# Kernel optimization log

Measured on AMD Instinct MI355X. Metric: run time of the kernel, lower is better.

Reference implementation:

```python
import jax, jax.numpy as jnp
import numpy as np

DIM = 1024
N_HEADS = 16
HEAD_DIM = DIM // N_HEADS
SCALE = HEAD_DIM ** -0.5


def setup_inputs() -> dict:
    key = jax.random.key(0)
    ks = jax.random.split(key, 5)
    B, N = 2, 2048
    x = jax.random.normal(ks[0], (B, N, DIM), dtype=jnp.float32)
    # torch Linear: y = x @ W.T + b, W shape (out, in)
    qkv_w = jax.random.normal(ks[1], (3 * DIM, DIM), dtype=jnp.float32) * (DIM ** -0.5)
    qkv_b = jax.random.normal(ks[2], (3 * DIM,), dtype=jnp.float32) * 0.02
    proj_w = jax.random.normal(ks[3], (DIM, DIM), dtype=jnp.float32) * (DIM ** -0.5)
    proj_b = jax.random.normal(ks[4], (DIM,), dtype=jnp.float32) * 0.02
    return {"x": x, "qkv_w": qkv_w, "qkv_b": qkv_b, "proj_w": proj_w, "proj_b": proj_b}


def reference(x, qkv_w, qkv_b, proj_w, proj_b):
    B, N, D = x.shape
    qkv = x @ qkv_w.T + qkv_b                      # [B, N, 3D]
    qkv = qkv.reshape(B, N, 3, N_HEADS, HEAD_DIM)
    qkv = jnp.transpose(qkv, (2, 0, 3, 1, 4))      # [3, B, H, N, hd]
    q, k, v = qkv[0], qkv[1], qkv[2]
    dp = jnp.einsum('bhqd,bhkd->bhqk', q, k) * SCALE  # [B, H, N, N]
    attn = jax.nn.softmax(dp, axis=-1)
    wa = jnp.einsum('bhqk,bhkd->bhqd', attn, v)    # [B, H, N, hd]
    wa = jnp.transpose(wa, (0, 2, 1, 3)).reshape(B, N, D)
    return wa @ proj_w.T + proj_b
```

## Files before the change

kernel.cpp:

```cpp
#include <hip/hip_runtime.h>

#define BATCH 2
#define SEQ   2048
#define DIM   1024
#define NHEAD 16
#define HD    64
#define BH    (BATCH * NHEAD)
#define SCALE 0.125f
#define LOG2E 1.44269504f
#define NT    (SEQ / 64)

typedef __attribute__((ext_vector_type(8))) short short8;
typedef __attribute__((ext_vector_type(4))) float f32x4;

#define MFMA16(a, b, c) __builtin_amdgcn_mfma_f32_16x16x32_bf16(a, b, c, 0, 0, 0)

__device__ __forceinline__ ushort f2bf(float f) {
    union { float f; unsigned u; } v;
    v.f = f;
    unsigned r = (v.u + 0x7FFF + ((v.u >> 16) & 1)) >> 16;
    return (ushort)r;
}

__device__ __forceinline__ uint4 ld8f_bf16(const float* p) {
    float4 f0 = *(const float4*)p;
    float4 f1 = *(const float4*)(p + 4);
    union { ushort us[8]; uint4 v; } u;
    u.us[0] = f2bf(f0.x); u.us[1] = f2bf(f0.y);
    u.us[2] = f2bf(f0.z); u.us[3] = f2bf(f0.w);
    u.us[4] = f2bf(f1.x); u.us[5] = f2bf(f1.y);
    u.us[6] = f2bf(f1.z); u.us[7] = f2bf(f1.w);
    return u.v;
}

__device__ __forceinline__ void gl_lds16(const ushort* g, ushort* l) {
    __builtin_amdgcn_global_load_lds(
        (const __attribute__((address_space(1))) unsigned int*)g,
        (__attribute__((address_space(3))) unsigned int*)l,
        16, 0, 0);
}

#define N_X  (BATCH * SEQ * DIM)
#define N_QW (3 * DIM * DIM)
#define N_PW (DIM * DIM)

__global__ __launch_bounds__(256) void cvt_kernel(
    const float* __restrict__ x, const float* __restrict__ qw,
    const float* __restrict__ pw, ushort* __restrict__ xb,
    ushort* __restrict__ qwb, ushort* __restrict__ pwb)
{
    const int i = (blockIdx.x * 256 + threadIdx.x) * 8;
    if (i < N_X)  *(uint4*)(xb  + i) = ld8f_bf16(x  + i);
    if (i < N_QW) *(uint4*)(qwb + i) = ld8f_bf16(qw + i);
    if (i < N_PW) *(uint4*)(pwb + i) = ld8f_bf16(pw + i);
}

template <int MODE, int WM, typename TOUT>
__global__ __launch_bounds__(256, 2) void gemm_bt(
    const ushort* __restrict__ A, const ushort* __restrict__ W,
    const float* __restrict__ bias, TOUT* __restrict__ out,
    int M, int Nout, int K)
{
    constexpr int BM = 2 * WM * 16;
    __shared__ __align__(16) ushort As[2][BM * 32];
    __shared__ __align__(16) ushort Bs[2][128 * 32];

    const int tid  = threadIdx.x;
    const int wave = tid >> 6, lane = tid & 63;
    const int quad = lane >> 4, l16 = lane & 15;
    const int wm = wave >> 1, wn = wave & 1;
    const int m0 = blockIdx.y * BM, n0 = blockIdx.x * 128;

    const int c0 = tid, c1 = tid + 256;
    const ushort* gA0 = A + (size_t)(m0 + (c0 >> 2)) * K + (c0 & 3) * 8;
    const ushort* gA1 = A + (size_t)(m0 + (c1 >> 2)) * K + (c1 & 3) * 8;
    const ushort* gB0 = W + (size_t)(n0 + (c0 >> 2)) * K + (c0 & 3) * 8;
    const ushort* gB1 = W + (size_t)(n0 + (c1 >> 2)) * K + (c1 & 3) * 8;

#define STAGE_G(buf, k0)                                                  \
    {                                                                     \
        gl_lds16(gA0 + (k0), &As[buf][(wave * 64) * 8]);                  \
        if (WM == 4) gl_lds16(gA1 + (k0), &As[buf][(wave * 64 + 256) * 8]); \
        gl_lds16(gB0 + (k0), &Bs[buf][(wave * 64) * 8]);                  \
        gl_lds16(gB1 + (k0), &Bs[buf][(wave * 64 + 256) * 8]);            \
    }

    f32x4 acc[WM][4];
#pragma unroll
    for (int i = 0; i < WM; i++)
#pragma unroll
        for (int j = 0; j < 4; j++) acc[i][j] = (f32x4){0.f, 0.f, 0.f, 0.f};

    const int KT = K >> 5;
    STAGE_G(0, 0)

    for (int kt = 0; kt < KT; kt++) {
        const int cur = kt & 1;
        __syncthreads();
        if (kt + 1 < KT) STAGE_G(cur ^ 1, (kt + 1) * 32)

        short8 af[WM], bfr[4];
#pragma unroll
        for (int mt = 0; mt < WM; mt++)
            af[mt] = *(const short8*)&As[cur][(wm * (WM * 16) + mt * 16 + l16) * 32 + quad * 8];
#pragma unroll
        for (int nt = 0; nt < 4; nt++)
            bfr[nt] = *(const short8*)&Bs[cur][(wn * 64 + nt * 16 + l16) * 32 + quad * 8];
#pragma unroll
        for (int mt = 0; mt < WM; mt++)
#pragma unroll
            for (int nt = 0; nt < 4; nt++)
                acc[mt][nt] = MFMA16(af[mt], bfr[nt], acc[mt][nt]);
    }

#pragma unroll
    for (int nt = 0; nt < 4; nt++) {
        const int n = n0 + wn * 64 + nt * 16 + l16;
        const float bv = bias[n];
#pragma unroll
        for (int mt = 0; mt < WM; mt++) {
            const int mBase = m0 + wm * (WM * 16) + mt * 16 + quad * 4;
#pragma unroll
            for (int r = 0; r < 4; r++) {
                const int m = mBase + r;
                float v = acc[mt][nt][r] + bv;
                if (MODE == 0) {
                    const int which = n >> 10, rem = n & 1023;
                    const int h = rem >> 6, d = rem & 63;
                    const int b = m >> 11, nq = m & 2047;
                    const int bh = b * NHEAD + h;
                    if (which == 0) v *= (SCALE * LOG2E);
                    size_t idx;
                    if (which == 2)
                        idx = (size_t)2 * BH * SEQ * HD + ((size_t)bh * HD + d) * SEQ + nq;
                    else
                        idx = (size_t)which * BH * SEQ * HD + ((size_t)bh * SEQ + nq) * HD + d;
                    ((ushort*)out)[idx] = f2bf(v);
                } else {
                    ((float*)out)[(size_t)m * Nout + n] = v;
                }
            }
        }
    }
#undef STAGE_G
}

#define PSTR 72

__global__ __launch_bounds__(512, 4) void attn_kernel(
    const ushort* __restrict__ qkv, ushort* __restrict__ wa)
{
    __shared__ __align__(16) ushort Ks[2][64 * 64];
    __shared__ __align__(16) ushort Vs[2][64 * 64];
    __shared__ __align__(16) ushort Pb[8][16 * PSTR];

    const int tid  = threadIdx.x;
    const int wave = tid >> 6, lane = tid & 63;
    const int quad = lane >> 4, l16 = lane & 15;

    const int l = blockIdx.x;
    const int bh = (l & 7) + 8 * (l >> 7);
    const int qi = (l >> 3) & 15;
    const int b = bh >> 4, h = bh & 15;

    const size_t hOff = (size_t)bh * SEQ * HD;
    const ushort* Q  = qkv + hOff;
    const ushort* Kg = qkv + (size_t)BH * SEQ * HD + hOff;
    const ushort* Vt = qkv + (size_t)2 * BH * SEQ * HD + hOff;
    const int q0 = qi * 128 + wave * 16;

    short8 aq0 = *(const short8*)&Q[(size_t)(q0 + l16) * HD + quad * 8];
    short8 aq1 = *(const short8*)&Q[(size_t)(q0 + l16) * HD + 32 + quad * 8];

    f32x4 o[4];
#pragma unroll
    for (int dt = 0; dt < 4; dt++) o[dt] = (f32x4){0.f, 0.f, 0.f, 0.f};
    float lsum[4];
#pragma unroll
    for (int r = 0; r < 4; r++) lsum[r] = 0.f;

    ushort* Pw = &Pb[wave][0];

    const int rr = lane >> 3;
    const int cc = ((lane & 7) ^ rr) * 8;
    const ushort* KgL = Kg + rr * HD + cc;
    const ushort* VtL = Vt + (size_t)rr * SEQ + cc;

#define STAGE(buf, kt)                                                       \
    {                                                                        \
        gl_lds16(KgL + (size_t)((kt) * 64 + wave * 8) * HD,                  \
                 &Ks[buf][wave * 512]);                                      \
        gl_lds16(VtL + (size_t)(wave * 8) * SEQ + (kt) * 64,                 \
                 &Vs[buf][wave * 512]);                                      \
    }

    STAGE(0, 0)

    const int sw  = (l16 & 7);
    const int ko0 = (quad ^ sw) * 8;
    const int ko1 = ko0 ^ 32;

    for (int kt = 0; kt < NT; kt++) {
        const int cur = kt & 1;
        __syncthreads();
        if (kt + 1 < NT) STAGE(cur ^ 1, kt + 1)

        f32x4 s[4];
#pragma unroll
        for (int t = 0; t < 4; t++) {
            const ushort* kb = &Ks[cur][(t * 16 + l16) * 64];
            short8 bk0 = *(const short8*)&kb[ko0];
            short8 bk1 = *(const short8*)&kb[ko1];
            f32x4 z = (f32x4){0.f, 0.f, 0.f, 0.f};
            z = MFMA16(aq0, bk0, z);
            z = MFMA16(aq1, bk1, z);
            s[t] = z;
        }

#pragma unroll
        for (int t = 0; t < 4; t++)
#pragma unroll
            for (int r = 0; r < 4; r++) {
                const float pv = __builtin_amdgcn_exp2f(s[t][r]);
                s[t][r] = pv;
                lsum[r] += pv;
            }

        short8 bv[4][2];
#pragma unroll
        for (int dt = 0; dt < 4; dt++) {
            const ushort* vb = &Vs[cur][(dt * 16 + l16) * 64];
            bv[dt][0] = *(const short8*)&vb[ko0];
            bv[dt][1] = *(const short8*)&vb[ko1];
        }

        __builtin_amdgcn_fence(__ATOMIC_ACQ_REL, "workgroup");
#pragma unroll
        for (int t = 0; t < 4; t++)
#pragma unroll
            for (int r = 0; r < 4; r++)
                Pw[(quad * 4 + r) * PSTR + l16 + t * 16] = f2bf(s[t][r]);
        __builtin_amdgcn_fence(__ATOMIC_ACQ_REL, "workgroup");

        short8 pa0 = *(const short8*)&Pw[l16 * PSTR + quad * 8];
        short8 pa1 = *(const short8*)&Pw[l16 * PSTR + 32 + quad * 8];

#pragma unroll
        for (int dt = 0; dt < 4; dt++) {
            o[dt] = MFMA16(pa0, bv[dt][0], o[dt]);
            o[dt] = MFMA16(pa1, bv[dt][1], o[dt]);
        }
    }

#pragma unroll
    for (int r = 0; r < 4; r++) {
        float ssum = lsum[r];
        ssum += __shfl_xor(ssum, 1);
        ssum += __shfl_xor(ssum, 2);
        ssum += __shfl_xor(ssum, 4);
        ssum += __shfl_xor(ssum, 8);
        lsum[r] = ssum;
    }

#pragma unroll
    for (int r = 0; r < 4; r++) {
        const float inv = 1.f / lsum[r];
        const int qrow = q0 + quad * 4 + r;
        ushort* dst = wa + ((size_t)(b * SEQ + qrow)) * DIM + h * HD;
#pragma unroll
        for (int dt = 0; dt < 4; dt++)
            dst[dt * 16 + l16] = f2bf(o[dt][r] * inv);
    }
}

extern "C" void kernel_launch(void* const* d_in, const int* in_sizes, int n_in,
                              void* d_out, int out_size, void* d_ws, size_t ws_size,
                              hipStream_t stream)
{
    const float* x      = (const float*)d_in[0];
    const float* qkv_w  = (const float*)d_in[1];
    const float* qkv_b  = (const float*)d_in[2];
    const float* proj_w = (const float*)d_in[3];
    const float* proj_b = (const float*)d_in[4];
    float* out = (float*)d_out;

    ushort* xb  = (ushort*)d_ws;
    ushort* qwb = xb  + (size_t)N_X;
    ushort* pwb = qwb + (size_t)N_QW;
    ushort* qkv = pwb + (size_t)N_PW;
    ushort* wa  = qkv + (size_t)3 * BH * SEQ * HD;

    const int M = BATCH * SEQ;
    dim3 blk(256);

    cvt_kernel<<<dim3((N_X / 8 + 255) / 256), blk, 0, stream>>>(
        x, qkv_w, proj_w, xb, qwb, pwb);

    gemm_bt<0, 4, ushort><<<dim3((3 * DIM) / 128, M / 128), blk, 0, stream>>>(
        xb, qwb, qkv_b, qkv, M, 3 * DIM, DIM);

    attn_kernel<<<dim3(512), dim3(512), 0, stream>>>(qkv, wa);

    gemm_bt<1, 2, float><<<dim3(DIM / 128, M / 64), blk, 0, stream>>>(
        wa, pwb, proj_b, out, M, DIM, DIM);
}
```

Measured before the change: 196.3 us.

## Rewrite attention with 32x32 MFMA, register-resident P via permlane swap

The attention kernel now computes transposed scores S^T = K·Q^T with 32x32x16 bf16 MFMAs, so each wave handles 32 query rows, and blocks shrink from 512 to 256 threads. The exponentiated probabilities are packed to bf16 in registers and rearranged with permlane32_swap to feed the PV MFMA directly. This removes the per-tile LDS round-trip for P and its fences. K/V tiles are staged 128 keys at a time, and s_setprio is placed around the MFMA bursts. The kernel keeps more accumulator registers live per wave and may run at lower occupancy.

```diff
diff --git a/kernel.cpp b/kernel.cpp
--- a/kernel.cpp
+++ b/kernel.cpp
@@ -8,12 +8,15 @@
 #define BH    (BATCH * NHEAD)
 #define SCALE 0.125f
 #define LOG2E 1.44269504f
-#define NT    (SEQ / 64)
+#define NT128 (SEQ / 128)
 
 typedef __attribute__((ext_vector_type(8))) short short8;
 typedef __attribute__((ext_vector_type(4))) float f32x4;
+typedef __attribute__((ext_vector_type(16))) float f32x16;
+typedef __attribute__((ext_vector_type(2))) unsigned int uint2v;
 
 #define MFMA16(a, b, c) __builtin_amdgcn_mfma_f32_16x16x32_bf16(a, b, c, 0, 0, 0)
+#define MFMA32(a, b, c) __builtin_amdgcn_mfma_f32_32x32x16_bf16(a, b, c, 0, 0, 0)
 
 __device__ __forceinline__ ushort f2bf(float f) {
     union { float f; unsigned u; } v;
@@ -145,132 +148,134 @@
 #undef STAGE_G
 }
 
-#define PSTR 72
-
-__global__ __launch_bounds__(512, 4) void attn_kernel(
+__global__ __launch_bounds__(256, 2) void attn_kernel(
     const ushort* __restrict__ qkv, ushort* __restrict__ wa)
 {
-    __shared__ __align__(16) ushort Ks[2][64 * 64];
-    __shared__ __align__(16) ushort Vs[2][64 * 64];
-    __shared__ __align__(16) ushort Pb[8][16 * PSTR];
+    __shared__ __align__(16) ushort Ks[2][2][64 * 64];
+    __shared__ __align__(16) ushort Vs[2][2][64 * 64];
 
     const int tid  = threadIdx.x;
     const int wave = tid >> 6, lane = tid & 63;
-    const int quad = lane >> 4, l16 = lane & 15;
+    const int l31  = lane & 31, hb = lane >> 5;
 
     const int l = blockIdx.x;
     const int bh = (l & 7) + 8 * (l >> 7);
     const int qi = (l >> 3) & 15;
-    const int b = bh >> 4, h = bh & 15;
+    const int b = bh >> 4, head = bh & 15;
 
     const size_t hOff = (size_t)bh * SEQ * HD;
     const ushort* Q  = qkv + hOff;
     const ushort* Kg = qkv + (size_t)BH * SEQ * HD + hOff;
     const ushort* Vt = qkv + (size_t)2 * BH * SEQ * HD + hOff;
-    const int q0 = qi * 128 + wave * 16;
-
-    short8 aq0 = *(const short8*)&Q[(size_t)(q0 + l16) * HD + quad * 8];
-    short8 aq1 = *(const short8*)&Q[(size_t)(q0 + l16) * HD + 32 + quad * 8];
-
-    f32x4 o[4];
-#pragma unroll
-    for (int dt = 0; dt < 4; dt++) o[dt] = (f32x4){0.f, 0.f, 0.f, 0.f};
-    float lsum[4];
-#pragma unroll
-    for (int r = 0; r < 4; r++) lsum[r] = 0.f;
-
-    ushort* Pw = &Pb[wave][0];
+    const int q0 = qi * 128 + wave * 32;
+
+    short8 qf[4];
+#pragma unroll
+    for (int i = 0; i < 4; i++)
+        qf[i] = *(const short8*)&Q[(size_t)(q0 + l31) * HD + i * 16 + hb * 8];
+
+    f32x16 o0, o1;
+#pragma unroll
+    for (int r = 0; r < 16; r++) { o0[r] = 0.f; o1[r] = 0.f; }
+    float lsum = 0.f;
 
     const int rr = lane >> 3;
     const int cc = ((lane & 7) ^ rr) * 8;
     const ushort* KgL = Kg + rr * HD + cc;
     const ushort* VtL = Vt + (size_t)rr * SEQ + cc;
 
-#define STAGE(buf, kt)                                                       \
-    {                                                                        \
-        gl_lds16(KgL + (size_t)((kt) * 64 + wave * 8) * HD,                  \
-                 &Ks[buf][wave * 512]);                                      \
-        gl_lds16(VtL + (size_t)(wave * 8) * SEQ + (kt) * 64,                 \
-                 &Vs[buf][wave * 512]);                                      \
+#define STAGE(buf, kt)                                                          \
+    {                                                                           \
+        const size_t kO = (size_t)(kt) * 128;                                   \
+        gl_lds16(KgL + (kO +      wave * 16    ) * HD, &Ks[buf][0][(wave*16    ) * 64]); \
+        gl_lds16(KgL + (kO +      wave * 16 + 8) * HD, &Ks[buf][0][(wave*16 + 8) * 64]); \
+        gl_lds16(KgL + (kO + 64 + wave * 16    ) * HD, &Ks[buf][1][(wave*16    ) * 64]); \
+        gl_lds16(KgL + (kO + 64 + wave * 16 + 8) * HD, &Ks[buf][1][(wave*16 + 8) * 64]); \
+        gl_lds16(VtL + (size_t)(wave*16    ) * SEQ + kO,      &Vs[buf][0][(wave*16    ) * 64]); \
+        gl_lds16(VtL + (size_t)(wave*16 + 8) * SEQ + kO,      &Vs[buf][0][(wave*16 + 8) * 64]); \
+        gl_lds16(VtL + (size_t)(wave*16    ) * SEQ + kO + 64, &Vs[buf][1][(wave*16    ) * 64]); \
+        gl_lds16(VtL + (size_t)(wave*16 + 8) * SEQ + kO + 64, &Vs[buf][1][(wave*16 + 8) * 64]); \
     }
 
     STAGE(0, 0)
 
-    const int sw  = (l16 & 7);
-    const int ko0 = (quad ^ sw) * 8;
-    const int ko1 = ko0 ^ 32;
-
-    for (int kt = 0; kt < NT; kt++) {
+    const int swz = l31 & 7;
+
+    for (int kt = 0; kt < NT128; kt++) {
         const int cur = kt & 1;
         __syncthreads();
-        if (kt + 1 < NT) STAGE(cur ^ 1, kt + 1)
-
-        f32x4 s[4];
-#pragma unroll
-        for (int t = 0; t < 4; t++) {
-            const ushort* kb = &Ks[cur][(t * 16 + l16) * 64];
-            short8 bk0 = *(const short8*)&kb[ko0];
-            short8 bk1 = *(const short8*)&kb[ko1];
-            f32x4 z = (f32x4){0.f, 0.f, 0.f, 0.f};
-            z = MFMA16(aq0, bk0, z);
-            z = MFMA16(aq1, bk1, z);
-            s[t] = z;
+        if (kt + 1 < NT128) STAGE(cur ^ 1, kt + 1)
+
+#pragma unroll
+        for (int hh = 0; hh < 2; hh++) {
+            const ushort* kb_ = &Ks[cur][hh][0];
+            const ushort* vb_ = &Vs[cur][hh][0];
+
+            f32x16 z[2];
+#pragma unroll
+            for (int kb = 0; kb < 2; kb++)
+#pragma unroll
+                for (int r = 0; r < 16; r++) z[kb][r] = 0.f;
+
+            __builtin_amdgcn_s_setprio(1);
+#pragma unroll
+            for (int i = 0; i < 4; i++) {
+                short8 ka0 = *(const short8*)&kb_[(l31     ) * 64 + (((2*i + hb) ^ swz) * 8)];
+                short8 ka1 = *(const short8*)&kb_[(32 + l31) * 64 + (((2*i + hb) ^ swz) * 8)];
+                z[0] = MFMA32(ka0, qf[i], z[0]);
+                z[1] = MFMA32(ka1, qf[i], z[1]);
+            }
+            __builtin_amdgcn_s_setprio(0);
+
+            unsigned u[2][8];
+#pragma unroll
+            for (int kb = 0; kb < 2; kb++) {
+#pragma unroll
+                for (int r = 0; r < 16; r++) {
+                    const float pv = __builtin_amdgcn_exp2f(z[kb][r]);
+                    z[kb][r] = pv;
+                    lsum += pv;
+                }
+#pragma unroll
+                for (int m = 0; m < 8; m++) {
+                    unsigned pk;
+                    asm("v_cvt_pk_bf16_f32 %0, %1, %2"
+                        : "=v"(pk) : "v"(z[kb][2*m]), "v"(z[kb][2*m + 1]));
+                    u[kb][m] = pk;
+                }
+            }
+
+            __builtin_amdgcn_s_setprio(1);
+#pragma unroll
+            for (int i = 0; i < 4; i++) {
+                const int kb = i >> 1, ii = i & 1;
+                uint2v s0 = __builtin_amdgcn_permlane32_swap(
+                    u[kb][4*ii + 0], u[kb][4*ii + 2], false, false);
+                uint2v s1 = __builtin_amdgcn_permlane32_swap(
+                    u[kb][4*ii + 1], u[kb][4*ii + 3], false, false);
+                union { unsigned w[4]; short8 s; } pf;
+                pf.w[0] = s0[0]; pf.w[1] = s1[0]; pf.w[2] = s0[1]; pf.w[3] = s1[1];
+                short8 vb0 = *(const short8*)&vb_[(l31     ) * 64 + (((2*i + hb) ^ swz) * 8)];
+                short8 vb1 = *(const short8*)&vb_[(32 + l31) * 64 + (((2*i + hb) ^ swz) * 8)];
+                o0 = MFMA32(pf.s, vb0, o0);
+                o1 = MFMA32(pf.s, vb1, o1);
+            }
+            __builtin_amdgcn_s_setprio(0);
         }
-
-#pragma unroll
-        for (int t = 0; t < 4; t++)
-#pragma unroll
-            for (int r = 0; r < 4; r++) {
-                const float pv = __builtin_amdgcn_exp2f(s[t][r]);
-                s[t][r] = pv;
-                lsum[r] += pv;
-            }
-
-        short8 bv[4][2];
-#pragma unroll
-        for (int dt = 0; dt < 4; dt++) {
-            const ushort* vb = &Vs[cur][(dt * 16 + l16) * 64];
-            bv[dt][0] = *(const short8*)&vb[ko0];
-            bv[dt][1] = *(const short8*)&vb[ko1];
-        }
-
-        __builtin_amdgcn_fence(__ATOMIC_ACQ_REL, "workgroup");
-#pragma unroll
-        for (int t = 0; t < 4; t++)
-#pragma unroll
-            for (int r = 0; r < 4; r++)
-                Pw[(quad * 4 + r) * PSTR + l16 + t * 16] = f2bf(s[t][r]);
-        __builtin_amdgcn_fence(__ATOMIC_ACQ_REL, "workgroup");
-
-        short8 pa0 = *(const short8*)&Pw[l16 * PSTR + quad * 8];
-        short8 pa1 = *(const short8*)&Pw[l16 * PSTR + 32 + quad * 8];
-
-#pragma unroll
-        for (int dt = 0; dt < 4; dt++) {
-            o[dt] = MFMA16(pa0, bv[dt][0], o[dt]);
-            o[dt] = MFMA16(pa1, bv[dt][1], o[dt]);
-        }
-    }
-
-#pragma unroll
-    for (int r = 0; r < 4; r++) {
-        float ssum = lsum[r];
-        ssum += __shfl_xor(ssum, 1);
-        ssum += __shfl_xor(ssum, 2);
-        ssum += __shfl_xor(ssum, 4);
-        ssum += __shfl_xor(ssum, 8);
-        lsum[r] = ssum;
-    }
-
-#pragma unroll
-    for (int r = 0; r < 4; r++) {
-        const float inv = 1.f / lsum[r];
-        const int qrow = q0 + quad * 4 + r;
-        ushort* dst = wa + ((size_t)(b * SEQ + qrow)) * DIM + h * HD;
-#pragma unroll
-        for (int dt = 0; dt < 4; dt++)
-            dst[dt * 16 + l16] = f2bf(o[dt][r] * inv);
-    }
+    }
+
+    lsum += __shfl_xor(lsum, 32);
+    const float invf = 1.f / lsum;
+
+#pragma unroll
+    for (int r = 0; r < 16; r++) {
+        const int qr = (r & 3) + 8 * (r >> 2) + 4 * hb;
+        const float iv = __shfl(invf, qr);
+        ushort* dst = wa + ((size_t)(b * SEQ + q0 + qr)) * DIM + head * HD + l31;
+        dst[0]  = f2bf(o0[r] * iv);
+        dst[32] = f2bf(o1[r] * iv);
+    }
+#undef STAGE
 }
 
 extern "C" void kernel_launch(void* const* d_in, const int* in_sizes, int n_in,
@@ -299,7 +304,7 @@
     gemm_bt<0, 4, ushort><<<dim3((3 * DIM) / 128, M / 128), blk, 0, stream>>>(
         xb, qwb, qkv_b, qkv, M, 3 * DIM, DIM);
 
-    attn_kernel<<<dim3(512), dim3(512), 0, stream>>>(qkv, wa);
+    attn_kernel<<<dim3(512), dim3(256), 0, stream>>>(qkv, wa);
 
     gemm_bt<1, 2, float><<<dim3(DIM / 128, M / 64), blk, 0, stream>>>(
         wa, pwb, proj_b, out, M, DIM, DIM);
```

New measurement: 186.1 us. 1.06x faster.
